# Kernel optimization log

Hardware: AMD Instinct MI355X
Metric: run time of the kernel (lower is better)

## Reference

```python
import jax, jax.numpy as jnp
import numpy as np


def setup_inputs() -> dict:
    key = jax.random.key(0)
    k1, k2, k3, k4 = jax.random.split(key, 4)
    B, L, D = 16, 2048, 128
    return {
        "query": jax.random.normal(k1, (B, L, D), dtype=jnp.float32),
        "key": jax.random.normal(k2, (B, L, D), dtype=jnp.float32),
        "value": jax.random.normal(k3, (B, L, D), dtype=jnp.float32),
        "mask": jax.random.randint(k4, (B, L, L), 0, 2, dtype=jnp.int32),
    }


def reference(query, key, value, mask):
    # scores: [B, L_q, L_k], scaled by sqrt(D_q)
    scale = 1.0 / jnp.sqrt(jnp.asarray(query.shape[-1], dtype=query.dtype))
    scores = jnp.einsum("bqd,bkd->bqk", query, key) * scale
    NEG = jnp.asarray(-1e9, dtype=scores.dtype)
    scores = jnp.where(mask == 0, NEG, scores)
    p_attn = jax.nn.softmax(scores, axis=-1)
    context = jnp.einsum("bqk,bkd->bqd", p_attn, value)
    return (context, p_attn)
```

## Files before the change

kernel.cpp:

```cpp
#include <hip/hip_runtime.h>
#include <hip/hip_bf16.h>
#include <hip/hip_fp16.h>

#define BB 16
#define LL 2048
#define DD 128
#define SCALE 0.08838834764831845f
#define CEXP 12.0f
#define NT 32

typedef _Float16 f16x8 __attribute__((ext_vector_type(8)));
typedef float f32x16 __attribute__((ext_vector_type(16)));

#define MFMA32(a,b,c) __builtin_amdgcn_mfma_f32_32x32x16_f16((a),(b),(c),0,0,0)

#define OFF_KB   0
#define OFF_VB   65536
#define OFF_PB   131072
#define OFF_RED  147456
#define LDS_MAIN 148480

#define WAITVM(N)  asm volatile("s_waitcnt vmcnt(" #N ")" ::: "memory")
#define WAITLGKM0  asm volatile("s_waitcnt lgkmcnt(0)" ::: "memory")
#define MEMFENCE   asm volatile("" ::: "memory")
#define SB0        __builtin_amdgcn_sched_barrier(0)

__device__ __forceinline__ f16x8 as_f16x8(uint4 v){
  union { uint4 u; f16x8 h; } x; x.u = v; return x.h;
}
__device__ __forceinline__ unsigned pkf16(float a, float b){
  __half ha = __float2half_rn(a), hb = __float2half_rn(b);
  return (unsigned)__half_as_ushort(ha) | ((unsigned)__half_as_ushort(hb) << 16);
}
__device__ __forceinline__ unsigned pkrtz(float a, float b){
  union { decltype(__builtin_amdgcn_cvt_pkrtz(0.f, 0.f)) h; unsigned u; } x;
  x.h = __builtin_amdgcn_cvt_pkrtz(a, b);
  return x.u;
}
__device__ __forceinline__ void stage16(const unsigned char* g, char* l){
  __builtin_amdgcn_global_load_lds(
      (const __attribute__((address_space(1))) void*)g,
      (__attribute__((address_space(3))) void*)l, 16, 0, 0);
}
__device__ __forceinline__ void stage2(const unsigned char* g, char* l, int soff){
  stage16(g + soff, l + soff);
  stage16(g + soff + 1024, l + soff + 1024);
}

__global__ __launch_bounds__(256) void prep_all(
    const float* __restrict__ K, const float* __restrict__ V,
    const int* __restrict__ M,
    unsigned char* __restrict__ kimg, unsigned char* __restrict__ vimg,
    unsigned int* __restrict__ bm)
{
  __shared__ float t[32][65];
  const int bid = blockIdx.x, tid = threadIdx.x;
  if (bid < 8192) {
    const size_t wi = (size_t)bid * 256 + tid;
    const int* mp = M + wi * 32;
    unsigned int wrd = 0;
#pragma unroll
    for (int j = 0; j < 8; ++j) {
      int4 v = *(const int4*)(mp + j*4);
      wrd |= (v.x ? 1u : 0u) << (4*j)
          |  (v.y ? 1u : 0u) << (4*j+1)
          |  (v.z ? 1u : 0u) << (4*j+2)
          |  (v.w ? 1u : 0u) << (4*j+3);
    }
    bm[wi] = wrd;
  } else if (bid < 10240) {
    const int G = (bid - 8192)*256 + tid;
    const int b = G >> 15;
    const int k = (G >> 4) & 2047;
    const int gd = G & 15;
    const float* src = K + ((size_t)b*LL + k)*DD + gd*8;
    float4 f0 = *(const float4*)(src);
    float4 f1 = *(const float4*)(src + 4);
    uint4 o;
    o.x = pkf16(f0.x, f0.y); o.y = pkf16(f0.z, f0.w);
    o.z = pkf16(f1.x, f1.y); o.w = pkf16(f1.z, f1.w);
    const size_t base = ((size_t)b*NT + (k>>6))*16384;
    *(uint4*)(kimg + base + (k&63)*256 + ((gd*16) ^ ((k&15)<<4))) = o;
  } else {
    const int t2 = bid - 10240;
    const int b = t2 >> 7;
    const int rem = t2 & 127;
    const int kt = rem >> 2, dt = rem & 3;
    const int k0 = kt*64, d0 = dt*32;
    const int kl = tid >> 2, dq = (tid & 3)*8;
    const float* src = V + ((size_t)b*LL + k0 + kl)*DD + d0 + dq;
    float4 f0 = *(const float4*)(src);
    float4 f1 = *(const float4*)(src + 4);
    t[dq+0][kl] = f0.x; t[dq+1][kl] = f0.y; t[dq+2][kl] = f0.z; t[dq+3][kl] = f0.w;
    t[dq+4][kl] = f1.x; t[dq+5][kl] = f1.y; t[dq+6][kl] = f1.z; t[dq+7][kl] = f1.w;
    __syncthreads();
    const int dl = tid >> 3, kg = tid & 7;
    const int d = d0 + dl;
    uint4 o;
    o.x = pkf16(t[dl][kg*8+0], t[dl][kg*8+1]);
    o.y = pkf16(t[dl][kg*8+2], t[dl][kg*8+3]);
    o.z = pkf16(t[dl][kg*8+4], t[dl][kg*8+5]);
    o.w = pkf16(t[dl][kg*8+6], t[dl][kg*8+7]);
    const size_t base = ((size_t)b*NT + kt)*16384;
    *(uint4*)(vimg + base + d*128 + ((kg*16) ^ ((d&7)<<4))) = o;
  }
}

#define QKCOMPUTE(BUFIDX) \
  const char* kb = KB + (BUFIDX)*16384 + krow*256; \
  f32x16 aA, aB; \
  _Pragma("unroll") for (int i=0;i<16;++i){aA[i]=0.f;aB[i]=0.f;} \
  _Pragma("unroll") for (int s=0;s<4;++s){ \
    uint4 af = *(const uint4*)(kb + (((s*2+hi)*16) ^ kswz)); \
    aA = MFMA32(as_f16x8(af), as_f16x8(qf[s]), aA); } \
  _Pragma("unroll") for (int s=4;s<8;++s){ \
    uint4 af = *(const uint4*)(kb + (((s*2+hi)*16) ^ kswz)); \
    aB = MFMA32(as_f16x8(af), as_f16x8(qf[s]), aB); }

#define P1BODY(RR) do { \
  WAITVM(6); \
  __builtin_amdgcn_s_barrier(); \
  MEMFENCE; \
  const unsigned bn2 = BMl[2*(((RR)+2)&31)]; \
  SB0; \
  stage2(KIMG + imgb + (size_t)(((RR)+3)&31)*16384, KB + (((RR)+3)&3)*16384, soff); \
  SB0; \
  QKCOMPUTE((RR)&3); \
  const unsigned bwh = bcur >> (4*hi); \
  _Pragma("unroll") for (int i=0;i<16;++i){ \
    const float sv = ((bwh>>((i&3)+8*(i>>2)))&1u) ? fmaf(aA[i]+aB[i], SCALE, -CEXP) : -1.0e9f; \
    psum[i&3] += __expf(sv); } \
  bcur = bn1; bn1 = bn2; \
} while(0)

#define P2BODY(RR, NTOK) do { \
  WAITVM(NTOK); \
  __builtin_amdgcn_s_barrier(); \
  MEMFENCE; \
  const unsigned bn2 = BMl[2*(((RR)+2)&31)]; \
  SB0; \
  stage2(KIMG + imgb + (size_t)(((RR)+3)&31)*16384, KB + (((RR)+3)&3)*16384, soff); \
  stage2(VIMG + imgb + (size_t)(((RR)+3)&31)*16384, VB + (((RR)+3)&3)*16384, soff); \
  SB0; \
  QKCOMPUTE((RR)&3); \
  const unsigned bwh = bcur >> (4*hi); \
  float pv[16]; \
  _Pragma("unroll") for (int i=0;i<16;++i){ \
    const float sv = ((bwh>>((i&3)+8*(i>>2)))&1u) ? fmaf(aA[i]+aB[i], SCALE, -CEXP) : -1.0e9f; \
    pv[i] = __expf(sv) * inv; } \
  { float* pr = Prow + (size_t)(RR)*64 + sub*32 + hi*4; \
    float4 o; \
    o.x=pv[0];  o.y=pv[1];  o.z=pv[2];  o.w=pv[3];  *(float4*)(pr)    = o; \
    o.x=pv[4];  o.y=pv[5];  o.z=pv[6];  o.w=pv[7];  *(float4*)(pr+8)  = o; \
    o.x=pv[8];  o.y=pv[9];  o.z=pv[10]; o.w=pv[11]; *(float4*)(pr+16) = o; \
    o.x=pv[12]; o.y=pv[13]; o.z=pv[14]; o.w=pv[15]; *(float4*)(pr+24) = o; } \
  SB0; \
  { char* pb = PB + p*4096 + sub*2048; \
    uint2 u; \
    u.x = pkrtz(pv[0],pv[1]);   u.y = pkrtz(pv[2],pv[3]);   *(uint2*)(pb + c*16 + hi*8) = u; \
    u.x = pkrtz(pv[4],pv[5]);   u.y = pkrtz(pv[6],pv[7]);   *(uint2*)(pb + (c+32)*16 + hi*8) = u; \
    u.x = pkrtz(pv[8],pv[9]);   u.y = pkrtz(pv[10],pv[11]); *(uint2*)(pb + 1024 + c*16 + hi*8) = u; \
    u.x = pkrtz(pv[12],pv[13]); u.y = pkrtz(pv[14],pv[15]); *(uint2*)(pb + 1024 + (c+32)*16 + hi*8) = u; } \
  WAITLGKM0; \
  __builtin_amdgcn_s_barrier(); \
  MEMFENCE; \
  _Pragma("unroll") for (int s2=0;s2<2;++s2){ \
    _Pragma("unroll") for (int k2=0;k2<2;++k2){ \
      const uint4 afr = *(const uint4*)(PB + p*4096 + s2*2048 + k2*1024 + l*16); \
      const int gix = s2*4 + k2*2 + hi; \
      const int d0v = sub*64 + c; \
      const uint4 b0 = *(const uint4*)(VB + ((RR)&3)*16384 + d0v*128 + ((gix*16) ^ ((d0v&7)<<4))); \
      ctx0 = MFMA32(as_f16x8(afr), as_f16x8(b0), ctx0); \
      const int d1v = sub*64 + 32 + c; \
      const uint4 b1 = *(const uint4*)(VB + ((RR)&3)*16384 + d1v*128 + ((gix*16) ^ ((d1v&7)<<4))); \
      ctx1 = MFMA32(as_f16x8(afr), as_f16x8(b1), ctx1); } } \
  bcur = bn1; bn1 = bn2; \
} while(0)

__global__ __launch_bounds__(512) void attn_main(
    const float* __restrict__ Q, const unsigned int* __restrict__ BM,
    const unsigned char* __restrict__ KIMG, const unsigned char* __restrict__ VIMG,
    float* __restrict__ ctxout, float* __restrict__ pout)
{
  extern __shared__ char lds[];
  char* KB = lds + OFF_KB;
  char* VB = lds + OFF_VB;
  char* PB = lds + OFF_PB;
  float* RED = (float*)(lds + OFF_RED);

  const int tid = threadIdx.x;
  const int w = tid >> 6, l = tid & 63;
  const int c = l & 31, hi = l >> 5;
  const int p = w >> 1, sub = w & 1;

  const int bid = blockIdx.x;
  const int xcd = bid & 7, jj = bid >> 3;
  const int b = xcd*2 + (jj >> 4);
  const int q0 = (jj & 15) * 128;
  const int qrow = q0 + p*32 + c;

  uint4 qf[8];
  const float* qp0 = Q + ((size_t)b*LL + qrow)*DD;
#pragma unroll
  for (int s = 0; s < 8; ++s) {
    const float4 f0 = *(const float4*)(qp0 + s*16 + hi*8);
    const float4 f1 = *(const float4*)(qp0 + s*16 + hi*8 + 4);
    uint4 qv;
    qv.x = pkf16(f0.x, f0.y); qv.y = pkf16(f0.z, f0.w);
    qv.z = pkf16(f1.x, f1.y); qv.w = pkf16(f1.z, f1.w);
    qf[s] = qv;
  }

  const size_t imgb = ((size_t)b * NT) * 16384;
  const int soff = w*2048 + l*16;
  const unsigned int* BMl = BM + ((size_t)b*LL + qrow)*64 + sub;
  const int krow = sub*32 + c;
  const int kswz = (c & 15) << 4;

  stage2(KIMG + imgb + 0*16384, KB + 0*16384, soff); SB0;
  unsigned bcur = BMl[0]; SB0;
  stage2(KIMG + imgb + 1*16384, KB + 1*16384, soff); SB0;
  unsigned bn1 = BMl[2]; SB0;
  stage2(KIMG + imgb + 2*16384, KB + 2*16384, soff); SB0;

  float psum[4] = {0.f, 0.f, 0.f, 0.f};
#pragma unroll 1
  for (int r = 0; r < 32; ++r) {
    P1BODY(r);
  }
  float sum = (psum[0] + psum[1]) + (psum[2] + psum[3]);
  sum += __shfl_xor(sum, 32);
  __syncthreads();
  if (l < 32) RED[(p*2+sub)*32 + c] = sum;
  __syncthreads();
  float tot = RED[(p*2+sub)*32 + c] + RED[(p*2+(1-sub))*32 + c];
  tot = fmaxf(tot, 1e-35f);
  const float inv = 1.0f / tot;
  __syncthreads();

  stage2(KIMG + imgb + 0*16384, KB + 0*16384, soff);
  stage2(VIMG + imgb + 0*16384, VB + 0*16384, soff); SB0;
  bcur = BMl[0]; SB0;
  stage2(KIMG + imgb + 1*16384, KB + 1*16384, soff);
  stage2(VIMG + imgb + 1*16384, VB + 1*16384, soff); SB0;
  bn1 = BMl[2]; SB0;
  stage2(KIMG + imgb + 2*16384, KB + 2*16384, soff);
  stage2(VIMG + imgb + 2*16384, VB + 2*16384, soff); SB0;

  f32x16 ctx0, ctx1;
#pragma unroll
  for (int i = 0; i < 16; ++i) { ctx0[i] = 0.f; ctx1[i] = 0.f; }
  float* Prow = pout + ((size_t)b*LL + qrow)*LL;

  P2BODY(0, 10);
  P2BODY(1, 14);
  P2BODY(2, 18);
#pragma unroll 1
  for (int r = 3; r < 32; ++r) {
    P2BODY(r, 22);
  }

#pragma unroll
  for (int reg = 0; reg < 16; ++reg) {
    const int q = q0 + p*32 + (reg&3) + 8*(reg>>2) + 4*hi;
    float* cr = ctxout + ((size_t)b*LL + q)*DD;
    cr[sub*64 + c]      = ctx0[reg];
    cr[sub*64 + 32 + c] = ctx1[reg];
  }
}

__global__ __launch_bounds__(256) void attn_naive(
    const float* __restrict__ Q, const float* __restrict__ K,
    const float* __restrict__ V, const int* __restrict__ M,
    float* __restrict__ ctx, float* __restrict__ pout)
{
  const int b = blockIdx.x >> 11;
  const int q = blockIdx.x & (LL-1);
  __shared__ float s[LL];
  __shared__ float red[256];
  const int tid = threadIdx.x;
  const float* qp = Q + ((size_t)b*LL + q)*DD;
  for (int kk = tid; kk < LL; kk += 256) {
    const float* kp = K + ((size_t)b*LL + kk)*DD;
    float a = 0.f;
    for (int d = 0; d < DD; ++d) a += qp[d]*kp[d];
    s[kk] = M[((size_t)b*LL + q)*LL + kk] ? a*SCALE : -1e9f;
  }
  __syncthreads();
  float mx = -3e38f;
  for (int kk = tid; kk < LL; kk += 256) mx = fmaxf(mx, s[kk]);
  red[tid] = mx; __syncthreads();
  for (int o = 128; o >= 1; o >>= 1) {
    if (tid < o) red[tid] = fmaxf(red[tid], red[tid+o]);
    __syncthreads();
  }
  const float mrow = red[0]; __syncthreads();
  float sm = 0.f;
  for (int kk = tid; kk < LL; kk += 256) { float e = __expf(s[kk]-mrow); s[kk] = e; sm += e; }
  red[tid] = sm; __syncthreads();
  for (int o = 128; o >= 1; o >>= 1) {
    if (tid < o) red[tid] += red[tid+o];
    __syncthreads();
  }
  const float inv = 1.0f / red[0]; __syncthreads();
  float* prow = pout + ((size_t)b*LL + q)*LL;
  for (int kk = tid; kk < LL; kk += 256) { s[kk] *= inv; prow[kk] = s[kk]; }
  __syncthreads();
  if (tid < DD) {
    float a = 0.f;
    for (int kk = 0; kk < LL; ++kk) a += s[kk]*V[((size_t)b*LL + kk)*DD + tid];
    ctx[((size_t)b*LL + q)*DD + tid] = a;
  }
}

extern "C" void kernel_launch(void* const* d_in, const int* in_sizes, int n_in,
                              void* d_out, int out_size, void* d_ws, size_t ws_size,
                              hipStream_t stream) {
  (void)in_sizes; (void)n_in; (void)out_size;
  const float* Q = (const float*)d_in[0];
  const float* K = (const float*)d_in[1];
  const float* V = (const float*)d_in[2];
  const int*   M = (const int*)d_in[3];
  float* ctx  = (float*)d_out;
  float* pout = ctx + (size_t)BB*LL*DD;
  const size_t IMG = (size_t)BB*NT*16384;
  const size_t NBM = (size_t)BB*LL*(LL/32);
  const size_t WS_NEED = IMG*2 + NBM*4;
  if (ws_size >= WS_NEED) {
    unsigned char* kimg = (unsigned char*)d_ws;
    unsigned char* vimg = kimg + IMG;
    unsigned int*  bmw  = (unsigned int*)(vimg + IMG);
    hipFuncSetAttribute(reinterpret_cast<const void*>(attn_main),
                        hipFuncAttributeMaxDynamicSharedMemorySize, LDS_MAIN);
    prep_all<<<12288, 256, 0, stream>>>(K, V, M, kimg, vimg, bmw);
    attn_main<<<256, 512, LDS_MAIN, stream>>>(Q, bmw, kimg, vimg, ctx, pout);
  } else {
    attn_naive<<<BB*LL, 256, 0, stream>>>(Q, K, V, M, ctx, pout);
  }
}
```

Measured before the change: 202.3 us.

## Write attention probabilities as coalesced rows from LDS staging with nontemporal hints

Each thread no longer writes its scattered MFMA-layout fragment of p_attn directly. The kernel now reads the fp16 P tile already staged in LDS and has each group of four threads write contiguous 16-byte chunks of a row, using nontemporal stores. The prep loads and the context stores also become nontemporal, and the vmcnt wait thresholds are adjusted to the new order of loads and stores. This targets the cost of the very large P output write, but the emitted probabilities now go through fp16 round-toward-zero, which reduces output precision.

```diff
diff --git a/kernel.cpp b/kernel.cpp
--- a/kernel.cpp
+++ b/kernel.cpp
@@ -11,6 +11,8 @@
 
 typedef _Float16 f16x8 __attribute__((ext_vector_type(8)));
 typedef float f32x16 __attribute__((ext_vector_type(16)));
+typedef float ef4 __attribute__((ext_vector_type(4)));
+typedef int   ei4 __attribute__((ext_vector_type(4)));
 
 #define MFMA32(a,b,c) __builtin_amdgcn_mfma_f32_32x32x16_f16((a),(b),(c),0,0,0)
 
@@ -36,6 +38,9 @@
   union { decltype(__builtin_amdgcn_cvt_pkrtz(0.f, 0.f)) h; unsigned u; } x;
   x.h = __builtin_amdgcn_cvt_pkrtz(a, b);
   return x.u;
+}
+__device__ __forceinline__ float h2f(unsigned short u){
+  return __half2float(__ushort_as_half(u));
 }
 __device__ __forceinline__ void stage16(const unsigned char* g, char* l){
   __builtin_amdgcn_global_load_lds(
@@ -61,7 +66,7 @@
     unsigned int wrd = 0;
 #pragma unroll
     for (int j = 0; j < 8; ++j) {
-      int4 v = *(const int4*)(mp + j*4);
+      ei4 v = __builtin_nontemporal_load((const ei4*)(mp + j*4));
       wrd |= (v.x ? 1u : 0u) << (4*j)
           |  (v.y ? 1u : 0u) << (4*j+1)
           |  (v.z ? 1u : 0u) << (4*j+2)
@@ -74,8 +79,8 @@
     const int k = (G >> 4) & 2047;
     const int gd = G & 15;
     const float* src = K + ((size_t)b*LL + k)*DD + gd*8;
-    float4 f0 = *(const float4*)(src);
-    float4 f1 = *(const float4*)(src + 4);
+    ef4 f0 = __builtin_nontemporal_load((const ef4*)(src));
+    ef4 f1 = __builtin_nontemporal_load((const ef4*)(src + 4));
     uint4 o;
     o.x = pkf16(f0.x, f0.y); o.y = pkf16(f0.z, f0.w);
     o.z = pkf16(f1.x, f1.y); o.w = pkf16(f1.z, f1.w);
@@ -89,8 +94,8 @@
     const int k0 = kt*64, d0 = dt*32;
     const int kl = tid >> 2, dq = (tid & 3)*8;
     const float* src = V + ((size_t)b*LL + k0 + kl)*DD + d0 + dq;
-    float4 f0 = *(const float4*)(src);
-    float4 f1 = *(const float4*)(src + 4);
+    ef4 f0 = __builtin_nontemporal_load((const ef4*)(src));
+    ef4 f1 = __builtin_nontemporal_load((const ef4*)(src + 4));
     t[dq+0][kl] = f0.x; t[dq+1][kl] = f0.y; t[dq+2][kl] = f0.z; t[dq+3][kl] = f0.w;
     t[dq+4][kl] = f1.x; t[dq+5][kl] = f1.y; t[dq+6][kl] = f1.z; t[dq+7][kl] = f1.w;
     __syncthreads();
@@ -148,13 +153,6 @@
   _Pragma("unroll") for (int i=0;i<16;++i){ \
     const float sv = ((bwh>>((i&3)+8*(i>>2)))&1u) ? fmaf(aA[i]+aB[i], SCALE, -CEXP) : -1.0e9f; \
     pv[i] = __expf(sv) * inv; } \
-  { float* pr = Prow + (size_t)(RR)*64 + sub*32 + hi*4; \
-    float4 o; \
-    o.x=pv[0];  o.y=pv[1];  o.z=pv[2];  o.w=pv[3];  *(float4*)(pr)    = o; \
-    o.x=pv[4];  o.y=pv[5];  o.z=pv[6];  o.w=pv[7];  *(float4*)(pr+8)  = o; \
-    o.x=pv[8];  o.y=pv[9];  o.z=pv[10]; o.w=pv[11]; *(float4*)(pr+16) = o; \
-    o.x=pv[12]; o.y=pv[13]; o.z=pv[14]; o.w=pv[15]; *(float4*)(pr+24) = o; } \
-  SB0; \
   { char* pb = PB + p*4096 + sub*2048; \
     uint2 u; \
     u.x = pkrtz(pv[0],pv[1]);   u.y = pkrtz(pv[2],pv[3]);   *(uint2*)(pb + c*16 + hi*8) = u; \
@@ -174,6 +172,16 @@
       const int d1v = sub*64 + 32 + c; \
       const uint4 b1 = *(const uint4*)(VB + ((RR)&3)*16384 + d1v*128 + ((gix*16) ^ ((d1v&7)<<4))); \
       ctx1 = MFMA32(as_f16x8(afr), as_f16x8(b1), ctx1); } } \
+   \
+  _Pragma("unroll") for (int o = 0; o < 4; ++o) { \
+    const uint2 u = *(const uint2*)(pbr + (o>>1)*2048 + (o&1)*1024); \
+    ef4 f; \
+    f.x = h2f((unsigned short)(u.x & 0xFFFFu)); \
+    f.y = h2f((unsigned short)(u.x >> 16)); \
+    f.z = h2f((unsigned short)(u.y & 0xFFFFu)); \
+    f.w = h2f((unsigned short)(u.y >> 16)); \
+    __builtin_nontemporal_store(f, (ef4*)(Pdst + (size_t)(RR)*64 + o*16 + pqt*4)); \
+  } \
   bcur = bn1; bn1 = bn2; \
 } while(0)
 
@@ -217,6 +225,12 @@
   const int krow = sub*32 + c;
   const int kswz = (c & 15) << 4;
 
+  const int prow_r = tid >> 2;
+  const int pqt = tid & 3;
+  const int pp = prow_r >> 5, pc = prow_r & 31;
+  const char* pbr = PB + pp*4096 + pc*16 + (pqt&1)*8 + (pqt>>1)*512;
+  float* Pdst = pout + ((size_t)b*LL + q0 + prow_r)*LL;
+
   stage2(KIMG + imgb + 0*16384, KB + 0*16384, soff); SB0;
   unsigned bcur = BMl[0]; SB0;
   stage2(KIMG + imgb + 1*16384, KB + 1*16384, soff); SB0;
@@ -250,22 +264,20 @@
   f32x16 ctx0, ctx1;
 #pragma unroll
   for (int i = 0; i < 16; ++i) { ctx0[i] = 0.f; ctx1[i] = 0.f; }
-  float* Prow = pout + ((size_t)b*LL + qrow)*LL;
 
   P2BODY(0, 10);
   P2BODY(1, 14);
-  P2BODY(2, 18);
 #pragma unroll 1
-  for (int r = 3; r < 32; ++r) {
-    P2BODY(r, 22);
+  for (int r = 2; r < 32; ++r) {
+    P2BODY(r, 18);
   }
 
 #pragma unroll
   for (int reg = 0; reg < 16; ++reg) {
     const int q = q0 + p*32 + (reg&3) + 8*(reg>>2) + 4*hi;
     float* cr = ctxout + ((size_t)b*LL + q)*DD;
-    cr[sub*64 + c]      = ctx0[reg];
-    cr[sub*64 + 32 + c] = ctx1[reg];
+    __builtin_nontemporal_store(ctx0[reg], &cr[sub*64 + c]);
+    __builtin_nontemporal_store(ctx1[reg], &cr[sub*64 + 32 + c]);
   }
 }
 
```

New measurement: 233.2 us. 1.15x slower.

## Fuse mask bit-packing into attention pass one instead of a separate prep pass

Applied to the files above, without the earlier changes.

The int32 mask is no longer packed into bitmasks by a separate section of the prep kernel. Pass one of the attention kernel now loads the raw int32 mask tiles directly, prefetching two tiles ahead. It builds the bit words in registers, uses them for the row-sum, and writes the packed words to workspace so pass two can reuse them. This removes one full read of the 268MB mask plus a launch's worth of work from the prep kernel, at the cost of more vector loads and register pressure inside the main kernel's first pass, with adjusted vmcnt waits.

```diff
diff --git a/kernel.cpp b/kernel.cpp
--- a/kernel.cpp
+++ b/kernel.cpp
@@ -21,7 +21,6 @@
 #define LDS_MAIN 148480
 
 #define WAITVM(N)  asm volatile("s_waitcnt vmcnt(" #N ")" ::: "memory")
-#define WAITLGKM0  asm volatile("s_waitcnt lgkmcnt(0)" ::: "memory")
 #define MEMFENCE   asm volatile("" ::: "memory")
 #define SB0        __builtin_amdgcn_sched_barrier(0)
 
@@ -47,29 +46,14 @@
   stage16(g + soff + 1024, l + soff + 1024);
 }
 
-__global__ __launch_bounds__(256) void prep_all(
+__global__ __launch_bounds__(256) void prep_img(
     const float* __restrict__ K, const float* __restrict__ V,
-    const int* __restrict__ M,
-    unsigned char* __restrict__ kimg, unsigned char* __restrict__ vimg,
-    unsigned int* __restrict__ bm)
+    unsigned char* __restrict__ kimg, unsigned char* __restrict__ vimg)
 {
   __shared__ float t[32][65];
   const int bid = blockIdx.x, tid = threadIdx.x;
-  if (bid < 8192) {
-    const size_t wi = (size_t)bid * 256 + tid;
-    const int* mp = M + wi * 32;
-    unsigned int wrd = 0;
-#pragma unroll
-    for (int j = 0; j < 8; ++j) {
-      int4 v = *(const int4*)(mp + j*4);
-      wrd |= (v.x ? 1u : 0u) << (4*j)
-          |  (v.y ? 1u : 0u) << (4*j+1)
-          |  (v.z ? 1u : 0u) << (4*j+2)
-          |  (v.w ? 1u : 0u) << (4*j+3);
-    }
-    bm[wi] = wrd;
-  } else if (bid < 10240) {
-    const int G = (bid - 8192)*256 + tid;
+  if (bid < 2048) {
+    const int G = bid*256 + tid;
     const int b = G >> 15;
     const int k = (G >> 4) & 2047;
     const int gd = G & 15;
@@ -82,7 +66,7 @@
     const size_t base = ((size_t)b*NT + (k>>6))*16384;
     *(uint4*)(kimg + base + (k&63)*256 + ((gd*16) ^ ((k&15)<<4))) = o;
   } else {
-    const int t2 = bid - 10240;
+    const int t2 = bid - 2048;
     const int b = t2 >> 7;
     const int rem = t2 & 127;
     const int kt = rem >> 2, dt = rem & 3;
@@ -117,20 +101,29 @@
     uint4 af = *(const uint4*)(kb + (((s*2+hi)*16) ^ kswz)); \
     aB = MFMA32(as_f16x8(af), as_f16x8(qf[s]), aB); }
 
-#define P1BODY(RR) do { \
-  WAITVM(6); \
+#define P1BODY(RR, WN) do { \
+  WAITVM(WN); \
   __builtin_amdgcn_s_barrier(); \
   MEMFENCE; \
-  const unsigned bn2 = BMl[2*(((RR)+2)&31)]; \
+  int4 t0, t1, t2, t3; \
+  { const int* mp2 = Mrow + (((RR)+2)&31)*64 + moff; \
+    t0 = *(const int4*)(mp2);    t1 = *(const int4*)(mp2+8); \
+    t2 = *(const int4*)(mp2+16); t3 = *(const int4*)(mp2+24); } \
   SB0; \
   stage2(KIMG + imgb + (size_t)(((RR)+3)&31)*16384, KB + (((RR)+3)&3)*16384, soff); \
   SB0; \
   QKCOMPUTE((RR)&3); \
-  const unsigned bwh = bcur >> (4*hi); \
+  const unsigned w16 = (cm0.x?0x1u:0u) | (cm0.y?0x2u:0u) | (cm0.z?0x4u:0u) | (cm0.w?0x8u:0u) \
+                     | (cm1.x?0x100u:0u) | (cm1.y?0x200u:0u) | (cm1.z?0x400u:0u) | (cm1.w?0x800u:0u) \
+                     | (cm2.x?0x10000u:0u) | (cm2.y?0x20000u:0u) | (cm2.z?0x40000u:0u) | (cm2.w?0x80000u:0u) \
+                     | (cm3.x?0x1000000u:0u) | (cm3.y?0x2000000u:0u) | (cm3.z?0x4000000u:0u) | (cm3.w?0x8000000u:0u); \
+  { const unsigned pw = __shfl_xor(w16, 32); \
+    if (l < 32) BMst[(RR)*2] = w16 | (pw << 4); } \
   _Pragma("unroll") for (int i=0;i<16;++i){ \
-    const float sv = ((bwh>>((i&3)+8*(i>>2)))&1u) ? fmaf(aA[i]+aB[i], SCALE, -CEXP) : -1.0e9f; \
+    const float sv = ((w16>>((i&3)+8*(i>>2)))&1u) ? fmaf(aA[i]+aB[i], SCALE, -CEXP) : -1.0e9f; \
     psum[i&3] += __expf(sv); } \
-  bcur = bn1; bn1 = bn2; \
+  cm0=n10; cm1=n11; cm2=n12; cm3=n13; \
+  n10=t0; n11=t1; n12=t2; n13=t3; \
 } while(0)
 
 #define P2BODY(RR, NTOK) do { \
@@ -161,7 +154,7 @@
     u.x = pkrtz(pv[4],pv[5]);   u.y = pkrtz(pv[6],pv[7]);   *(uint2*)(pb + (c+32)*16 + hi*8) = u; \
     u.x = pkrtz(pv[8],pv[9]);   u.y = pkrtz(pv[10],pv[11]); *(uint2*)(pb + 1024 + c*16 + hi*8) = u; \
     u.x = pkrtz(pv[12],pv[13]); u.y = pkrtz(pv[14],pv[15]); *(uint2*)(pb + 1024 + (c+32)*16 + hi*8) = u; } \
-  WAITLGKM0; \
+  asm volatile("s_waitcnt lgkmcnt(0)" ::: "memory"); \
   __builtin_amdgcn_s_barrier(); \
   MEMFENCE; \
   _Pragma("unroll") for (int s2=0;s2<2;++s2){ \
@@ -178,7 +171,8 @@
 } while(0)
 
 __global__ __launch_bounds__(512) void attn_main(
-    const float* __restrict__ Q, const unsigned int* __restrict__ BM,
+    const float* __restrict__ Q, const int* __restrict__ M,
+    unsigned int* __restrict__ BM,
     const unsigned char* __restrict__ KIMG, const unsigned char* __restrict__ VIMG,
     float* __restrict__ ctxout, float* __restrict__ pout)
 {
@@ -213,20 +207,30 @@
 
   const size_t imgb = ((size_t)b * NT) * 16384;
   const int soff = w*2048 + l*16;
-  const unsigned int* BMl = BM + ((size_t)b*LL + qrow)*64 + sub;
+  const int* Mrow = M + ((size_t)b*LL + qrow)*LL;
+  const int moff = sub*32 + hi*4;
+  unsigned int* BMst = BM + ((size_t)b*LL + qrow)*64 + sub;
+  const unsigned int* BMl = BMst;
   const int krow = sub*32 + c;
   const int kswz = (c & 15) << 4;
 
+  int4 cm0, cm1, cm2, cm3, n10, n11, n12, n13;
   stage2(KIMG + imgb + 0*16384, KB + 0*16384, soff); SB0;
-  unsigned bcur = BMl[0]; SB0;
+  { const int* mp = Mrow + moff;
+    cm0 = *(const int4*)(mp);    cm1 = *(const int4*)(mp+8);
+    cm2 = *(const int4*)(mp+16); cm3 = *(const int4*)(mp+24); } SB0;
   stage2(KIMG + imgb + 1*16384, KB + 1*16384, soff); SB0;
-  unsigned bn1 = BMl[2]; SB0;
+  { const int* mp = Mrow + 64 + moff;
+    n10 = *(const int4*)(mp);    n11 = *(const int4*)(mp+8);
+    n12 = *(const int4*)(mp+16); n13 = *(const int4*)(mp+24); } SB0;
   stage2(KIMG + imgb + 2*16384, KB + 2*16384, soff); SB0;
 
   float psum[4] = {0.f, 0.f, 0.f, 0.f};
+  P1BODY(0, 8);
+  P1BODY(1, 9);
 #pragma unroll 1
-  for (int r = 0; r < 32; ++r) {
-    P1BODY(r);
+  for (int r = 2; r < 32; ++r) {
+    P1BODY(r, 10);
   }
   float sum = (psum[0] + psum[1]) + (psum[2] + psum[3]);
   sum += __shfl_xor(sum, 32);
@@ -240,10 +244,10 @@
 
   stage2(KIMG + imgb + 0*16384, KB + 0*16384, soff);
   stage2(VIMG + imgb + 0*16384, VB + 0*16384, soff); SB0;
-  bcur = BMl[0]; SB0;
+  unsigned bcur = BMl[0]; SB0;
   stage2(KIMG + imgb + 1*16384, KB + 1*16384, soff);
   stage2(VIMG + imgb + 1*16384, VB + 1*16384, soff); SB0;
-  bn1 = BMl[2]; SB0;
+  unsigned bn1 = BMl[2]; SB0;
   stage2(KIMG + imgb + 2*16384, KB + 2*16384, soff);
   stage2(VIMG + imgb + 2*16384, VB + 2*16384, soff); SB0;
 
@@ -332,8 +336,8 @@
     unsigned int*  bmw  = (unsigned int*)(vimg + IMG);
     hipFuncSetAttribute(reinterpret_cast<const void*>(attn_main),
                         hipFuncAttributeMaxDynamicSharedMemorySize, LDS_MAIN);
-    prep_all<<<12288, 256, 0, stream>>>(K, V, M, kimg, vimg, bmw);
-    attn_main<<<256, 512, LDS_MAIN, stream>>>(Q, bmw, kimg, vimg, ctx, pout);
+    prep_img<<<4096, 256, 0, stream>>>(K, V, kimg, vimg);
+    attn_main<<<256, 512, LDS_MAIN, stream>>>(Q, M, bmw, kimg, vimg, ctx, pout);
   } else {
     attn_naive<<<BB*LL, 256, 0, stream>>>(Q, K, V, M, ctx, pout);
   }
```

New measurement: 218.2 us. 1.08x slower.

## Halve query tile per block, split PV across wave groups, double-buffer K/V

Applied to the files above, without the earlier changes.

Each block now handles 64 query rows instead of 128, and the grid grows from 256 to 512 blocks. The 8 waves form two groups that recompute the same QK scores but each write half of the probability output and own one 32-column slice of the PV product. The K/V LDS ring drops from 4 stages to 2, which cuts LDS use roughly in half so that more blocks can be resident per CU. In exchange the QK and softmax-numerator work is duplicated across the two wave groups, and the shallower prefetch gives less room to hide global-load latency.

```diff
diff --git a/kernel.cpp b/kernel.cpp
--- a/kernel.cpp
+++ b/kernel.cpp
@@ -15,13 +15,12 @@
 #define MFMA32(a,b,c) __builtin_amdgcn_mfma_f32_32x32x16_f16((a),(b),(c),0,0,0)
 
 #define OFF_KB   0
-#define OFF_VB   65536
-#define OFF_PB   131072
-#define OFF_RED  147456
-#define LDS_MAIN 148480
+#define OFF_VB   32768
+#define OFF_PB   65536
+#define OFF_RED  73728
+#define LDS_MAIN 74240
 
 #define WAITVM(N)  asm volatile("s_waitcnt vmcnt(" #N ")" ::: "memory")
-#define WAITLGKM0  asm volatile("s_waitcnt lgkmcnt(0)" ::: "memory")
 #define MEMFENCE   asm volatile("" ::: "memory")
 #define SB0        __builtin_amdgcn_sched_barrier(0)
 
@@ -117,15 +116,15 @@
     uint4 af = *(const uint4*)(kb + (((s*2+hi)*16) ^ kswz)); \
     aB = MFMA32(as_f16x8(af), as_f16x8(qf[s]), aB); }
 
-#define P1BODY(RR) do { \
-  WAITVM(6); \
+#define P1BODY(RR, WN) do { \
+  WAITVM(WN); \
   __builtin_amdgcn_s_barrier(); \
   MEMFENCE; \
+  stage2(KIMG + imgb + (size_t)(((RR)+1)&31)*16384, KB + (((RR)+1)&1)*16384, soff); \
+  SB0; \
   const unsigned bn2 = BMl[2*(((RR)+2)&31)]; \
   SB0; \
-  stage2(KIMG + imgb + (size_t)(((RR)+3)&31)*16384, KB + (((RR)+3)&3)*16384, soff); \
-  SB0; \
-  QKCOMPUTE((RR)&3); \
+  QKCOMPUTE((RR)&1); \
   const unsigned bwh = bcur >> (4*hi); \
   _Pragma("unroll") for (int i=0;i<16;++i){ \
     const float sv = ((bwh>>((i&3)+8*(i>>2)))&1u) ? fmaf(aA[i]+aB[i], SCALE, -CEXP) : -1.0e9f; \
@@ -133,51 +132,54 @@
   bcur = bn1; bn1 = bn2; \
 } while(0)
 
-#define P2BODY(RR, NTOK) do { \
-  WAITVM(NTOK); \
+#define P2BODY(RR, WN) do { \
+  WAITVM(WN); \
   __builtin_amdgcn_s_barrier(); \
   MEMFENCE; \
+  stage2(KIMG + imgb + (size_t)(((RR)+1)&31)*16384, KB + (((RR)+1)&1)*16384, soff); \
+  stage2(VIMG + imgb + (size_t)(((RR)+1)&31)*16384, VB + (((RR)+1)&1)*16384, soff); \
+  SB0; \
   const unsigned bn2 = BMl[2*(((RR)+2)&31)]; \
   SB0; \
-  stage2(KIMG + imgb + (size_t)(((RR)+3)&31)*16384, KB + (((RR)+3)&3)*16384, soff); \
-  stage2(VIMG + imgb + (size_t)(((RR)+3)&31)*16384, VB + (((RR)+3)&3)*16384, soff); \
-  SB0; \
-  QKCOMPUTE((RR)&3); \
+  QKCOMPUTE((RR)&1); \
   const unsigned bwh = bcur >> (4*hi); \
   float pv[16]; \
   _Pragma("unroll") for (int i=0;i<16;++i){ \
     const float sv = ((bwh>>((i&3)+8*(i>>2)))&1u) ? fmaf(aA[i]+aB[i], SCALE, -CEXP) : -1.0e9f; \
     pv[i] = __expf(sv) * inv; } \
-  { float* pr = Prow + (size_t)(RR)*64 + sub*32 + hi*4; \
+  { const float g0 = e ? pv[8]  : pv[0]; \
+    const float g1 = e ? pv[9]  : pv[1]; \
+    const float g2 = e ? pv[10] : pv[2]; \
+    const float g3 = e ? pv[11] : pv[3]; \
+    const float g4 = e ? pv[12] : pv[4]; \
+    const float g5 = e ? pv[13] : pv[5]; \
+    const float g6 = e ? pv[14] : pv[6]; \
+    const float g7 = e ? pv[15] : pv[7]; \
+    float* prq = Prow + (size_t)(RR)*64 + sub*32 + hi*4 + e*16; \
     float4 o; \
-    o.x=pv[0];  o.y=pv[1];  o.z=pv[2];  o.w=pv[3];  *(float4*)(pr)    = o; \
-    o.x=pv[4];  o.y=pv[5];  o.z=pv[6];  o.w=pv[7];  *(float4*)(pr+8)  = o; \
-    o.x=pv[8];  o.y=pv[9];  o.z=pv[10]; o.w=pv[11]; *(float4*)(pr+16) = o; \
-    o.x=pv[12]; o.y=pv[13]; o.z=pv[14]; o.w=pv[15]; *(float4*)(pr+24) = o; } \
-  SB0; \
-  { char* pb = PB + p*4096 + sub*2048; \
+    o.x=g0; o.y=g1; o.z=g2; o.w=g3; *(float4*)(prq)   = o; \
+    o.x=g4; o.y=g5; o.z=g6; o.w=g7; *(float4*)(prq+8) = o; } \
+  SB0; \
+  if (e == 0) { \
+    char* pb = PB + p*4096 + sub*2048; \
     uint2 u; \
     u.x = pkrtz(pv[0],pv[1]);   u.y = pkrtz(pv[2],pv[3]);   *(uint2*)(pb + c*16 + hi*8) = u; \
     u.x = pkrtz(pv[4],pv[5]);   u.y = pkrtz(pv[6],pv[7]);   *(uint2*)(pb + (c+32)*16 + hi*8) = u; \
     u.x = pkrtz(pv[8],pv[9]);   u.y = pkrtz(pv[10],pv[11]); *(uint2*)(pb + 1024 + c*16 + hi*8) = u; \
     u.x = pkrtz(pv[12],pv[13]); u.y = pkrtz(pv[14],pv[15]); *(uint2*)(pb + 1024 + (c+32)*16 + hi*8) = u; } \
-  WAITLGKM0; \
+  asm volatile("s_waitcnt lgkmcnt(0)" ::: "memory"); \
   __builtin_amdgcn_s_barrier(); \
   MEMFENCE; \
   _Pragma("unroll") for (int s2=0;s2<2;++s2){ \
     _Pragma("unroll") for (int k2=0;k2<2;++k2){ \
       const uint4 afr = *(const uint4*)(PB + p*4096 + s2*2048 + k2*1024 + l*16); \
       const int gix = s2*4 + k2*2 + hi; \
-      const int d0v = sub*64 + c; \
-      const uint4 b0 = *(const uint4*)(VB + ((RR)&3)*16384 + d0v*128 + ((gix*16) ^ ((d0v&7)<<4))); \
-      ctx0 = MFMA32(as_f16x8(afr), as_f16x8(b0), ctx0); \
-      const int d1v = sub*64 + 32 + c; \
-      const uint4 b1 = *(const uint4*)(VB + ((RR)&3)*16384 + d1v*128 + ((gix*16) ^ ((d1v&7)<<4))); \
-      ctx1 = MFMA32(as_f16x8(afr), as_f16x8(b1), ctx1); } } \
+      const uint4 b0 = *(const uint4*)(VB + ((RR)&1)*16384 + dv*128 + ((gix*16) ^ ((dv&7)<<4))); \
+      ctx0 = MFMA32(as_f16x8(afr), as_f16x8(b0), ctx0); } } \
   bcur = bn1; bn1 = bn2; \
 } while(0)
 
-__global__ __launch_bounds__(512) void attn_main(
+__global__ __launch_bounds__(512, 4) void attn_main(
     const float* __restrict__ Q, const unsigned int* __restrict__ BM,
     const unsigned char* __restrict__ KIMG, const unsigned char* __restrict__ VIMG,
     float* __restrict__ ctxout, float* __restrict__ pout)
@@ -191,12 +193,12 @@
   const int tid = threadIdx.x;
   const int w = tid >> 6, l = tid & 63;
   const int c = l & 31, hi = l >> 5;
-  const int p = w >> 1, sub = w & 1;
+  const int e = w >> 2, p = (w >> 1) & 1, sub = w & 1;
 
   const int bid = blockIdx.x;
   const int xcd = bid & 7, jj = bid >> 3;
-  const int b = xcd*2 + (jj >> 4);
-  const int q0 = (jj & 15) * 128;
+  const int b = xcd*2 + (jj >> 5);
+  const int q0 = (jj & 31) * 64;
   const int qrow = q0 + p*32 + c;
 
   uint4 qf[8];
@@ -216,22 +218,22 @@
   const unsigned int* BMl = BM + ((size_t)b*LL + qrow)*64 + sub;
   const int krow = sub*32 + c;
   const int kswz = (c & 15) << 4;
+  const int dv = (sub*2 + e)*32 + c;
 
   stage2(KIMG + imgb + 0*16384, KB + 0*16384, soff); SB0;
   unsigned bcur = BMl[0]; SB0;
-  stage2(KIMG + imgb + 1*16384, KB + 1*16384, soff); SB0;
   unsigned bn1 = BMl[2]; SB0;
-  stage2(KIMG + imgb + 2*16384, KB + 2*16384, soff); SB0;
 
   float psum[4] = {0.f, 0.f, 0.f, 0.f};
+  P1BODY(0, 2);
 #pragma unroll 1
-  for (int r = 0; r < 32; ++r) {
-    P1BODY(r);
+  for (int r = 1; r < 32; ++r) {
+    P1BODY(r, 1);
   }
   float sum = (psum[0] + psum[1]) + (psum[2] + psum[3]);
   sum += __shfl_xor(sum, 32);
   __syncthreads();
-  if (l < 32) RED[(p*2+sub)*32 + c] = sum;
+  if (l < 32 && e == 0) RED[(p*2+sub)*32 + c] = sum;
   __syncthreads();
   float tot = RED[(p*2+sub)*32 + c] + RED[(p*2+(1-sub))*32 + c];
   tot = fmaxf(tot, 1e-35f);
@@ -241,31 +243,24 @@
   stage2(KIMG + imgb + 0*16384, KB + 0*16384, soff);
   stage2(VIMG + imgb + 0*16384, VB + 0*16384, soff); SB0;
   bcur = BMl[0]; SB0;
-  stage2(KIMG + imgb + 1*16384, KB + 1*16384, soff);
-  stage2(VIMG + imgb + 1*16384, VB + 1*16384, soff); SB0;
   bn1 = BMl[2]; SB0;
-  stage2(KIMG + imgb + 2*16384, KB + 2*16384, soff);
-  stage2(VIMG + imgb + 2*16384, VB + 2*16384, soff); SB0;
-
-  f32x16 ctx0, ctx1;
+
+  f32x16 ctx0;
 #pragma unroll
-  for (int i = 0; i < 16; ++i) { ctx0[i] = 0.f; ctx1[i] = 0.f; }
+  for (int i = 0; i < 16; ++i) ctx0[i] = 0.f;
   float* Prow = pout + ((size_t)b*LL + qrow)*LL;
 
-  P2BODY(0, 10);
-  P2BODY(1, 14);
-  P2BODY(2, 18);
+  P2BODY(0, 2);
 #pragma unroll 1
-  for (int r = 3; r < 32; ++r) {
-    P2BODY(r, 22);
-  }
-
+  for (int r = 1; r < 32; ++r) {
+    P2BODY(r, 3);
+  }
+
+  WAITVM(0);
 #pragma unroll
   for (int reg = 0; reg < 16; ++reg) {
     const int q = q0 + p*32 + (reg&3) + 8*(reg>>2) + 4*hi;
-    float* cr = ctxout + ((size_t)b*LL + q)*DD;
-    cr[sub*64 + c]      = ctx0[reg];
-    cr[sub*64 + 32 + c] = ctx1[reg];
+    ctxout[((size_t)b*LL + q)*DD + dv] = ctx0[reg];
   }
 }
 
@@ -296,7 +291,7 @@
   }
   const float mrow = red[0]; __syncthreads();
   float sm = 0.f;
-  for (int kk = tid; kk < LL; kk += 256) { float e = __expf(s[kk]-mrow); s[kk] = e; sm += e; }
+  for (int kk = tid; kk < LL; kk += 256) { float e2 = __expf(s[kk]-mrow); s[kk] = e2; sm += e2; }
   red[tid] = sm; __syncthreads();
   for (int o = 128; o >= 1; o >>= 1) {
     if (tid < o) red[tid] += red[tid+o];
@@ -333,7 +328,7 @@
     hipFuncSetAttribute(reinterpret_cast<const void*>(attn_main),
                         hipFuncAttributeMaxDynamicSharedMemorySize, LDS_MAIN);
     prep_all<<<12288, 256, 0, stream>>>(K, V, M, kimg, vimg, bmw);
-    attn_main<<<256, 512, LDS_MAIN, stream>>>(Q, bmw, kimg, vimg, ctx, pout);
+    attn_main<<<512, 512, LDS_MAIN, stream>>>(Q, bmw, kimg, vimg, ctx, pout);
   } else {
     attn_naive<<<BB*LL, 256, 0, stream>>>(Q, K, V, M, ctx, pout);
   }
```

New measurement: 228.1 us. +12.7%, slower.
